# Optimization experiments

Measured on AMD Instinct MI355X. Metric: run time of the kernel, lower is better.

Reference implementation:

```python
import jax, jax.numpy as jnp
import numpy as np

N, D_IN, D_OUT = 128, 512, 512
B = 256

def setup_inputs() -> dict:
    key = jax.random.key(0)
    kx, kw, kb = jax.random.split(key, 3)
    x = jax.random.normal(kx, (B, N, D_IN), dtype=jnp.float32)
    # nn.Linear default init: uniform(-1/sqrt(d_in), 1/sqrt(d_in)) for weight and bias
    bound = 1.0 / np.sqrt(D_IN)
    weight = jax.random.uniform(kw, (N, D_IN, D_OUT), dtype=jnp.float32, minval=-bound, maxval=bound)
    bias = jax.random.uniform(kb, (N, D_OUT), dtype=jnp.float32, minval=-bound, maxval=bound)
    return {"x": x, "weight": weight, "bias": bias}

def reference(x, weight, bias):
    # per-position linear: out[b,n,o] = sum_i x[b,n,i] * W[n,i,o] + bias[n,o]
    out = jnp.einsum('bni,nio->bno', x, weight)
    return out + bias[None]
```

## Files before the change

### kernel.cpp

```cpp
#include <hip/hip_runtime.h>

typedef __attribute__((ext_vector_type(8))) __bf16 bf16x8;
typedef __attribute__((ext_vector_type(4))) __bf16 bf16x4;
typedef __attribute__((ext_vector_type(4))) float f32x4;
typedef __attribute__((ext_vector_type(2))) float f32x2;

#define DI 512
#define DO 512
#define XROW (128 * DI)
#define OROW (128 * DO)
#define BK 32
#define BOFF 8192
#define BUFSZ 16384

#define LGKM0()  asm volatile("s_waitcnt lgkmcnt(0)" ::: "memory")
#define SBAR()   __builtin_amdgcn_s_barrier()
#define SCHED0() __builtin_amdgcn_sched_barrier(0)

__global__ __launch_bounds__(512, 6)
void nlinear_mfma(const float* __restrict__ xp, const float* __restrict__ wp,
                  const float* __restrict__ bp, float* __restrict__ op) {
  int blk = blockIdx.x;
  int L = ((blk & 7) << 7) + (blk >> 3);
  int n = L >> 3, mt = (L >> 2) & 1, ot = L & 3;
  int mBase = mt << 7, oBase = ot << 7;

  __shared__ char lds[2 * BUFSZ];

  int tid = threadIdx.x, lane = tid & 63, wid = tid >> 6;
  int wm = (wid >> 2) << 6, wn = (wid & 3) << 5;
  int l16 = lane & 15, l4 = lane >> 4;

  int arow = tid >> 2, aks = tid & 3;
  const float* aSrc = xp + (size_t)(mBase + arow) * XROW + n * DI + aks * 8;
  int aWr = arow * 64 + ((aks ^ ((arow >> 1) & 3)) << 4);

  f32x4 aRv[2];
  auto loadA = [&](int kt) {
    aRv[0] = *(const f32x4*)(aSrc + kt * BK);
    aRv[1] = *(const f32x4*)(aSrc + kt * BK + 4);
  };
  auto writeA = [&](int bufOff) {
    bf16x8 v;
    #pragma unroll
    for (int e = 0; e < 8; ++e) v[e] = (__bf16)aRv[e >> 2][e & 3];
    *(bf16x8*)(lds + bufOff + aWr) = v;
  };

  int bo2 = (tid & 63) << 1, bkg = tid >> 6;
  const float* bSrc = wp + ((size_t)n * DI + (bkg << 2)) * DO + oBase + bo2;
  int bslotx = ((bkg >> 1) << 4) ;
  int bhalf = (bkg & 1) << 3;
  int bWr0 = BOFF + (bo2)     * 64 + ((bslotx) ^ (((bo2 >> 1) & 3) << 4)) + bhalf;
  int bWr1 = BOFF + (bo2 + 1) * 64 + ((bslotx) ^ (((bo2 >> 1) & 3) << 4)) + bhalf;

  f32x2 bRv[4];
  auto loadB = [&](int kt) {
    #pragma unroll
    for (int j = 0; j < 4; ++j)
      bRv[j] = *(const f32x2*)(bSrc + (size_t)(kt * BK + j) * DO);
  };
  auto writeB = [&](int bufOff) {
    bf16x4 v0, v1;
    #pragma unroll
    for (int j = 0; j < 4; ++j) { v0[j] = (__bf16)bRv[j].x; v1[j] = (__bf16)bRv[j].y; }
    *(bf16x4*)(lds + bufOff + bWr0) = v0;
    *(bf16x4*)(lds + bufOff + bWr1) = v1;
  };

  f32x4 acc[4][2];
  #pragma unroll
  for (int i = 0; i < 4; ++i)
    #pragma unroll
    for (int j = 0; j < 2; ++j)
      acc[i][j] = f32x4{0.f, 0.f, 0.f, 0.f};

  bf16x8 bfr[2];
  auto loadBfr = [&](int bufOff) {
    #pragma unroll
    for (int j = 0; j < 2; ++j) {
      int row = wn + j * 16 + l16;
      int slot = l4 ^ ((row >> 1) & 3);
      bfr[j] = *(const bf16x8*)(lds + bufOff + BOFF + row * 64 + slot * 16);
    }
  };
  auto computeI = [&](int bufOff, int i) {
    int row = wm + i * 16 + l16;
    int slot = l4 ^ ((row >> 1) & 3);
    bf16x8 af = *(const bf16x8*)(lds + bufOff + row * 64 + slot * 16);
    acc[i][0] = __builtin_amdgcn_mfma_f32_16x16x32_bf16(af, bfr[0], acc[i][0], 0, 0, 0);
    acc[i][1] = __builtin_amdgcn_mfma_f32_16x16x32_bf16(af, bfr[1], acc[i][1], 0, 0, 0);
  };

  float bi[2];
  #pragma unroll
  for (int j = 0; j < 2; ++j)
    bi[j] = bp[n * DO + oBase + wn + j * 16 + l16];

  loadA(0); loadB(0);
  writeA(0); writeB(0);
  loadA(1); loadB(1);
  SCHED0(); LGKM0(); SBAR(); SCHED0();

  for (int kt = 0; kt < 16; ++kt) {
    int cur = (kt & 1) * BUFSZ, nxt = cur ^ BUFSZ;
    if (kt < 15) { writeA(nxt); writeB(nxt); }
    if (kt < 14) { loadA(kt + 2); loadB(kt + 2); }
    SCHED0();
    loadBfr(cur);
    computeI(cur, 0);
    computeI(cur, 1);
    computeI(cur, 2);
    computeI(cur, 3);
    if (kt < 15) { SCHED0(); LGKM0(); SBAR(); SCHED0(); }
  }

  #pragma unroll
  for (int i = 0; i < 4; ++i) {
    #pragma unroll
    for (int j = 0; j < 2; ++j) {
      #pragma unroll
      for (int r = 0; r < 4; ++r) {
        int m = mBase + wm + i * 16 + l4 * 4 + r;
        int o = oBase + wn + j * 16 + l16;
        op[(size_t)m * OROW + n * DO + o] = acc[i][j][r] + bi[j];
      }
    }
  }
}

extern "C" void kernel_launch(void* const* d_in, const int* in_sizes, int n_in,
                              void* d_out, int out_size, void* d_ws, size_t ws_size,
                              hipStream_t stream) {
  const float* x = (const float*)d_in[0];
  const float* w = (const float*)d_in[1];
  const float* b = (const float*)d_in[2];
  float* o = (float*)d_out;
  hipLaunchKernelGGL(nlinear_mfma, dim3(1024), dim3(512), 0, stream, x, w, b, o);
}
```

Before: 49.25 us.

## Double K tile to 64 with 8-slot swizzle and halve barrier count

Raises the K tile from 32 to 64, doubling the LDS buffers to 64KB total and using an 8-slot XOR swizzle with 128-byte rows. The main loop drops from 16 to 8 iterations, so there are half as many barriers and waitcnt stalls per block, and global loads become wider. In exchange, each thread needs more registers for prefetch and LDS use per block rises, so launch bounds fall from 6 to 4 blocks, which can reduce occupancy.

Result: slower. 51.92 us (+5.4%).

```diff
diff --git a/kernel.cpp b/kernel.cpp
--- a/kernel.cpp
+++ b/kernel.cpp
@@ -1,7 +1,6 @@
 #include <hip/hip_runtime.h>
 
 typedef __attribute__((ext_vector_type(8))) __bf16 bf16x8;
-typedef __attribute__((ext_vector_type(4))) __bf16 bf16x4;
 typedef __attribute__((ext_vector_type(4))) float f32x4;
 typedef __attribute__((ext_vector_type(2))) float f32x2;
 
@@ -9,15 +8,15 @@
 #define DO 512
 #define XROW (128 * DI)
 #define OROW (128 * DO)
-#define BK 32
-#define BOFF 8192
-#define BUFSZ 16384
+#define BK 64
+#define BOFF 16384
+#define BUFSZ 32768
 
 #define LGKM0()  asm volatile("s_waitcnt lgkmcnt(0)" ::: "memory")
 #define SBAR()   __builtin_amdgcn_s_barrier()
 #define SCHED0() __builtin_amdgcn_sched_barrier(0)
 
-__global__ __launch_bounds__(512, 6)
+__global__ __launch_bounds__(512, 4)
 void nlinear_mfma(const float* __restrict__ xp, const float* __restrict__ wp,
                   const float* __restrict__ bp, float* __restrict__ op) {
   int blk = blockIdx.x;
@@ -31,41 +30,47 @@
   int wm = (wid >> 2) << 6, wn = (wid & 3) << 5;
   int l16 = lane & 15, l4 = lane >> 4;
 
-  int arow = tid >> 2, aks = tid & 3;
-  const float* aSrc = xp + (size_t)(mBase + arow) * XROW + n * DI + aks * 8;
-  int aWr = arow * 64 + ((aks ^ ((arow >> 1) & 3)) << 4);
 
-  f32x4 aRv[2];
+  int arow = tid >> 2, aq = tid & 3;
+  const float* aSrc = xp + (size_t)(mBase + arow) * XROW + n * DI + aq * 16;
+  int aswz = ((arow >> 1) & 7) << 4;
+  int aWr0 = arow * 128 + (((aq << 1))     << 4 ^ aswz);
+  int aWr1 = arow * 128 + (((aq << 1) | 1) << 4 ^ aswz);
+
+  f32x4 aRv[4];
   auto loadA = [&](int kt) {
-    aRv[0] = *(const f32x4*)(aSrc + kt * BK);
-    aRv[1] = *(const f32x4*)(aSrc + kt * BK + 4);
+    #pragma unroll
+    for (int i = 0; i < 4; ++i)
+      aRv[i] = *(const f32x4*)(aSrc + kt * BK + i * 4);
   };
   auto writeA = [&](int bufOff) {
-    bf16x8 v;
+    bf16x8 v0, v1;
     #pragma unroll
-    for (int e = 0; e < 8; ++e) v[e] = (__bf16)aRv[e >> 2][e & 3];
-    *(bf16x8*)(lds + bufOff + aWr) = v;
+    for (int e = 0; e < 8; ++e) {
+      v0[e] = (__bf16)aRv[e >> 2][e & 3];
+      v1[e] = (__bf16)aRv[2 + (e >> 2)][e & 3];
+    }
+    *(bf16x8*)(lds + bufOff + aWr0) = v0;
+    *(bf16x8*)(lds + bufOff + aWr1) = v1;
   };
 
-  int bo2 = (tid & 63) << 1, bkg = tid >> 6;
-  const float* bSrc = wp + ((size_t)n * DI + (bkg << 2)) * DO + oBase + bo2;
-  int bslotx = ((bkg >> 1) << 4) ;
-  int bhalf = (bkg & 1) << 3;
-  int bWr0 = BOFF + (bo2)     * 64 + ((bslotx) ^ (((bo2 >> 1) & 3) << 4)) + bhalf;
-  int bWr1 = BOFF + (bo2 + 1) * 64 + ((bslotx) ^ (((bo2 >> 1) & 3) << 4)) + bhalf;
+  int bo2 = (tid & 63) << 1, boct = tid >> 6;
+  const float* bSrc = wp + ((size_t)n * DI + (boct << 3)) * DO + oBase + bo2;
+  int bWr0 = BOFF + (bo2)     * 128 + ((boct ^ (((bo2)     >> 1) & 7)) << 4);
+  int bWr1 = BOFF + (bo2 + 1) * 128 + ((boct ^ (((bo2 + 1) >> 1) & 7)) << 4);
 
-  f32x2 bRv[4];
+  f32x2 bRv[8];
   auto loadB = [&](int kt) {
     #pragma unroll
-    for (int j = 0; j < 4; ++j)
+    for (int j = 0; j < 8; ++j)
       bRv[j] = *(const f32x2*)(bSrc + (size_t)(kt * BK + j) * DO);
   };
   auto writeB = [&](int bufOff) {
-    bf16x4 v0, v1;
+    bf16x8 v0, v1;
     #pragma unroll
-    for (int j = 0; j < 4; ++j) { v0[j] = (__bf16)bRv[j].x; v1[j] = (__bf16)bRv[j].y; }
-    *(bf16x4*)(lds + bufOff + bWr0) = v0;
-    *(bf16x4*)(lds + bufOff + bWr1) = v1;
+    for (int j = 0; j < 8; ++j) { v0[j] = (__bf16)bRv[j].x; v1[j] = (__bf16)bRv[j].y; }
+    *(bf16x8*)(lds + bufOff + bWr0) = v0;
+    *(bf16x8*)(lds + bufOff + bWr1) = v1;
   };
 
   f32x4 acc[4][2];
@@ -75,21 +80,25 @@
     for (int j = 0; j < 2; ++j)
       acc[i][j] = f32x4{0.f, 0.f, 0.f, 0.f};
 
-  bf16x8 bfr[2];
-  auto loadBfr = [&](int bufOff) {
+  auto compute = [&](int bufOff) {
     #pragma unroll
-    for (int j = 0; j < 2; ++j) {
-      int row = wn + j * 16 + l16;
-      int slot = l4 ^ ((row >> 1) & 3);
-      bfr[j] = *(const bf16x8*)(lds + bufOff + BOFF + row * 64 + slot * 16);
+    for (int ks = 0; ks < 2; ++ks) {
+      bf16x8 bfr[2];
+      #pragma unroll
+      for (int j = 0; j < 2; ++j) {
+        int row = wn + j * 16 + l16;
+        int slot = (ks * 4 + l4) ^ ((row >> 1) & 7);
+        bfr[j] = *(const bf16x8*)(lds + bufOff + BOFF + row * 128 + slot * 16);
+      }
+      #pragma unroll
+      for (int i = 0; i < 4; ++i) {
+        int row = wm + i * 16 + l16;
+        int slot = (ks * 4 + l4) ^ ((row >> 1) & 7);
+        bf16x8 af = *(const bf16x8*)(lds + bufOff + row * 128 + slot * 16);
+        acc[i][0] = __builtin_amdgcn_mfma_f32_16x16x32_bf16(af, bfr[0], acc[i][0], 0, 0, 0);
+        acc[i][1] = __builtin_amdgcn_mfma_f32_16x16x32_bf16(af, bfr[1], acc[i][1], 0, 0, 0);
+      }
     }
-  };
-  auto computeI = [&](int bufOff, int i) {
-    int row = wm + i * 16 + l16;
-    int slot = l4 ^ ((row >> 1) & 3);
-    bf16x8 af = *(const bf16x8*)(lds + bufOff + row * 64 + slot * 16);
-    acc[i][0] = __builtin_amdgcn_mfma_f32_16x16x32_bf16(af, bfr[0], acc[i][0], 0, 0, 0);
-    acc[i][1] = __builtin_amdgcn_mfma_f32_16x16x32_bf16(af, bfr[1], acc[i][1], 0, 0, 0);
   };
 
   float bi[2];
@@ -102,17 +111,17 @@
   loadA(1); loadB(1);
   SCHED0(); LGKM0(); SBAR(); SCHED0();
 
-  for (int kt = 0; kt < 16; ++kt) {
+  for (int kt = 0; kt < 8; ++kt) {
     int cur = (kt & 1) * BUFSZ, nxt = cur ^ BUFSZ;
-    if (kt < 15) { writeA(nxt); writeB(nxt); }
-    if (kt < 14) { loadA(kt + 2); loadB(kt + 2); }
-    SCHED0();
-    loadBfr(cur);
-    computeI(cur, 0);
-    computeI(cur, 1);
-    computeI(cur, 2);
-    computeI(cur, 3);
-    if (kt < 15) { SCHED0(); LGKM0(); SBAR(); SCHED0(); }
+    if (kt < 7) {
+      writeA(nxt);
+      if (kt < 6) loadA(kt + 2);
+      writeB(nxt);
+      if (kt < 6) loadB(kt + 2);
+      SCHED0();
+    }
+    compute(cur);
+    if (kt < 7) { SCHED0(); LGKM0(); SBAR(); SCHED0(); }
   }
 
   #pragma unroll
```
